# Kernel optimization log

Measured on AMD Instinct MI355X. Metric: run time of the kernel, lower is better.

The kernel has to match this reference:

```python
import jax, jax.numpy as jnp
import numpy as np

N = 50000      # nodes
E = 800000     # edges (avg degree 16)
IN = 256       # in_feats
H = 128        # hidden_feats
C = 40         # out_feats == num classes (label dim)
LPA_ITERS = 10


def setup_inputs() -> dict:
    key = jax.random.key(0)
    ks = jax.random.split(key, 9)
    features = jax.random.normal(ks[0], (N, IN), dtype=jnp.float32)
    labels = jax.random.normal(ks[1], (N, C), dtype=jnp.float32)
    mask = jax.random.randint(ks[2], (N,), 0, 2) > 0          # bool [N]
    src = jax.random.randint(ks[3], (E,), 0, N, dtype=jnp.int32)
    dst = jax.random.randint(ks[4], (E,), 0, N, dtype=jnp.int32)
    W1 = jax.random.normal(ks[5], (IN, H), dtype=jnp.float32) * (1.0 / np.sqrt(IN))
    b1 = jnp.zeros((H,), dtype=jnp.float32)
    W2 = jax.random.normal(ks[6], (H, C), dtype=jnp.float32) * (1.0 / np.sqrt(H))
    b2 = jnp.zeros((C,), dtype=jnp.float32)
    return {"features": features, "labels": labels, "mask": mask,
            "src": src, "dst": dst, "W1": W1, "b1": b1, "W2": W2, "b2": b2}


def reference(features, labels, mask, src, dst, W1, b1, W2, b2):
    ones_e = jnp.ones((E,), dtype=jnp.float32)
    deg_out = jax.ops.segment_sum(ones_e, src, num_segments=N)  # out-degree
    deg_in = jax.ops.segment_sum(ones_e, dst, num_segments=N)   # in-degree
    norm_src = jnp.maximum(deg_out, 1.0) ** -0.5                 # DGL clamps deg>=1
    norm_dst = jnp.maximum(deg_in, 1.0) ** -0.5

    def gconv(x, W, b):
        # DGL GraphConv, norm='both': D_in^{-1/2} A^T D_out^{-1/2} (x W) + b
        h = (x @ W) * norm_src[:, None]                          # [N, d_out]
        agg = jax.ops.segment_sum(h[src], dst, num_segments=N)   # gather+scatter-add
        return agg * norm_dst[:, None] + b

    x = jax.nn.relu(gconv(features, W1, b1))
    # dropout identity in eval mode
    x = gconv(x, W2, b2)

    # Label propagation: adj[src,dst]=1 so (adj @ y)[i] = sum_{(i->j)} y[j]
    masked_labels = jnp.where(mask[:, None], labels, 0.0)

    def step(y, _):
        y = jax.ops.segment_sum(y[dst], src, num_segments=N)
        y = jnp.where(mask[:, None], labels, y)
        return y, None

    y, _ = jax.lax.scan(step, masked_labels, None, length=LPA_ITERS)
    return x, y
```

## Files before the change

kernel.cpp:

```cpp
#include <hip/hip_runtime.h>

#define Nn 50000
#define Ee 800000
#define INF_ 256
#define HID 128
#define NC 40
#define CAPD 48
#define CAPS 48
#define LPA_ITERS 10
#define NB 98
#define BSH 9
#define EPB 1024
#define NBLK ((Ee + EPB - 1) / EPB)
#define G1_ROWS 64
#define G1BLK ((Nn + G1_ROWS - 1) / G1_ROWS)
#define CAPB_D 10240
#define CAPB_S 6144

typedef __attribute__((ext_vector_type(8))) short bfrag;
typedef __attribute__((ext_vector_type(4))) float ffrag;

__device__ inline unsigned f2bf2(float a, float b) {
    unsigned ua = __float_as_uint(a); ua += 0x7FFFu + ((ua >> 16) & 1u);
    unsigned ub = __float_as_uint(b); ub += 0x7FFFu + ((ub >> 16) & 1u);
    return (ua >> 16) | (ub & 0xFFFF0000u);
}
__device__ inline unsigned short f2bf(float a) {
    unsigned ua = __float_as_uint(a); ua += 0x7FFFu + ((ua >> 16) & 1u);
    return (unsigned short)(ua >> 16);
}
__device__ inline float bf_lo(unsigned u) { return __uint_as_float(u << 16); }
__device__ inline float bf_hi(unsigned u) { return __uint_as_float(u & 0xFFFF0000u); }

__global__ void detect_fmt(const unsigned int* __restrict__ m, int* flag) {
    int i = blockIdx.x * blockDim.x + threadIdx.x;
    if (i < 12500) {
        if (m[i] > 1u) atomicOr(flag, 1);
    }
}

__device__ inline bool read_mask(const void* mask, int node, int fmt) {
    if (fmt) return ((const unsigned char*)mask)[node] != 0;
    return ((const int*)mask)[node] != 0;
}

__global__ void prep_w1t(const float* __restrict__ W1,
                         unsigned short* __restrict__ W1t) {
    int c = blockIdx.x;
    int k = threadIdx.x;
    W1t[c * INF_ + k] = f2bf(W1[(size_t)k * HID + c]);
}

__global__ __launch_bounds__(256) void phase1(
    const int* __restrict__ src, const int* __restrict__ dst,
    const void* __restrict__ mask, const int* __restrict__ flag,
    int* __restrict__ cnt_src, int* __restrict__ cur_d, int* __restrict__ cur_s,
    unsigned* __restrict__ bkt_d, unsigned* __restrict__ bkt_s,
    const float* __restrict__ feat, const unsigned short* __restrict__ W1t,
    unsigned short* __restrict__ h1b) {
    __shared__ uint4 smem[784];
    const int tid = threadIdx.x;
    if (blockIdx.x < NBLK) {
        unsigned* stage_d = (unsigned*)smem;
        unsigned* stage_s = stage_d + EPB;
        int* hd  = (int*)(stage_s + EPB);
        int* od  = hd + NB;
        int* cd  = od + NB + 1;
        int* gd_ = cd + NB;
        int* hs  = gd_ + NB;
        int* os_ = hs + NB;
        int* cs_ = os_ + NB + 1;
        int* gs_ = cs_ + NB;
        int lane = tid & 63;
        int wid = tid >> 6;
        int e0 = blockIdx.x * EPB;
        int fmt = *flag;
        if (tid < NB) { hd[tid] = 0; hs[tid] = 0; }
        __syncthreads();

        int rs[EPB / 256], rd[EPB / 256];
        unsigned um = 0;
#pragma unroll
        for (int k = 0; k < EPB / 256; k++) {
            int e = e0 + tid + k * 256;
            rs[k] = -1; rd[k] = -1;
            if (e < Ee) {
                int s = src[e], d = dst[e];
                rs[k] = s; rd[k] = d;
                atomicAdd(&cnt_src[s], 1);
                atomicAdd(&hd[d >> BSH], 1);
                if (!read_mask(mask, s, fmt)) {
                    um |= (1u << k);
                    atomicAdd(&hs[s >> BSH], 1);
                }
            }
        }
        __syncthreads();
        if (wid < 2) {
            int* h = wid ? hs : hd;
            int* o = wid ? os_ : od;
            int i0 = lane * 2;
            int v0 = (i0 < NB) ? h[i0] : 0;
            int v1 = (i0 + 1 < NB) ? h[i0 + 1] : 0;
            int s = v0 + v1;
#pragma unroll
            for (int d = 1; d < 64; d <<= 1) {
                int t = __shfl_up(s, d);
                if (lane >= d) s += t;
            }
            int excl = s - v0 - v1;
            if (i0 < NB) o[i0] = excl;
            if (i0 + 1 < NB) o[i0 + 1] = excl + v0;
            if (lane == 63) o[NB] = s;
        }
        __syncthreads();
        if (tid < NB) {
            gd_[tid] = hd[tid] ? atomicAdd(&cur_d[tid], hd[tid]) : 0;
            gs_[tid] = hs[tid] ? atomicAdd(&cur_s[tid], hs[tid]) : 0;
            cd[tid] = od[tid];
            cs_[tid] = os_[tid];
        }
        __syncthreads();
#pragma unroll
        for (int k = 0; k < EPB / 256; k++) {
            if (rd[k] >= 0) {
                int p = atomicAdd(&cd[rd[k] >> BSH], 1);
                stage_d[p] = ((unsigned)rd[k] << 16) | (unsigned)rs[k];
                if (um & (1u << k)) {
                    int q = atomicAdd(&cs_[rs[k] >> BSH], 1);
                    stage_s[q] = ((unsigned)rs[k] << 16) | (unsigned)rd[k];
                }
            }
        }
        __syncthreads();
        for (int b = wid; b < NB; b += 4) {
            int base = od[b], cntb = hd[b], g0 = gd_[b];
            unsigned* gb = bkt_d + (size_t)b * CAPB_D;
            for (int i = lane; i < cntb; i += 64) {
                int pos = g0 + i;
                if (pos < CAPB_D) gb[pos] = stage_d[base + i];
            }
            int bs = os_[b], cnts = hs[b], gs0 = gs_[b];
            unsigned* gbs = bkt_s + (size_t)b * CAPB_S;
            for (int i = lane; i < cnts; i += 64) {
                int pos = gs0 + i;
                if (pos < CAPB_S) gbs[pos] = stage_s[bs + i];
            }
        }
    } else {
        unsigned short* lA = (unsigned short*)smem;
        unsigned short* lB = lA + G1_ROWS * 32;
        const int row0 = (blockIdx.x - NBLK) * G1_ROWS;
        const int w = tid >> 6;
        const int l = tid & 63;
        const int lane15 = l & 15;
        const int quad = l >> 4;
        const int rw0 = w * 16;

        ffrag acc[8];
#pragma unroll
        for (int t = 0; t < 8; t++) acc[t] = (ffrag){0.f, 0.f, 0.f, 0.f};

        for (int k0 = 0; k0 < INF_; k0 += 32) {
#pragma unroll
            for (int p = 0; p < 2; p++) {
                int idx = tid + p * 256;
                int r = idx >> 3, c4 = idx & 7;
                int grow = row0 + r;
                float4 v = make_float4(0.f, 0.f, 0.f, 0.f);
                if (grow < Nn)
                    v = *(const float4*)(feat + (size_t)grow * INF_ + k0 + c4 * 4);
                uint2 pk;
                pk.x = f2bf2(v.x, v.y);
                pk.y = f2bf2(v.z, v.w);
                *(uint2*)((char*)lA + r * 64 + c4 * 8) = pk;
            }
#pragma unroll
            for (int p = 0; p < 2; p++) {
                int idx = tid + p * 256;
                int col = idx >> 2, q = idx & 3;
                uint4 v = *(const uint4*)((const char*)W1t + col * 512 + k0 * 2 + q * 16);
                *(uint4*)((char*)lB + col * 64 + q * 16) = v;
            }
            __syncthreads();
            int arow = rw0 + lane15;
            bfrag af = *(const bfrag*)((const char*)lA + arow * 64 + quad * 16);
#pragma unroll
            for (int t = 0; t < 8; t++) {
                int col = t * 16 + lane15;
                bfrag bf = *(const bfrag*)((const char*)lB + col * 64 + quad * 16);
                acc[t] = __builtin_amdgcn_mfma_f32_16x16x32_bf16(af, bf, acc[t], 0, 0, 0);
            }
            __syncthreads();
        }
#pragma unroll
        for (int t = 0; t < 8; t++) {
#pragma unroll
            for (int i = 0; i < 4; i++) {
                int grow = row0 + rw0 + quad * 4 + i;
                if (grow < Nn)
                    h1b[(size_t)grow * HID + t * 16 + lane15] = f2bf(acc[t][i]);
            }
        }
    }
}

__global__ __launch_bounds__(256) void build_csr_both(
    const unsigned* __restrict__ bkt_d, const int* __restrict__ cur_d,
    const unsigned* __restrict__ bkt_s, const int* __restrict__ cur_s,
    const void* __restrict__ mask, const int* __restrict__ flag,
    const int* __restrict__ cnt_src,
    int* __restrict__ adj_dst, int* __restrict__ cnt_dst,
    int* __restrict__ adj_s, int* __restrict__ cnt_u, int* __restrict__ cnt_m,
    float* __restrict__ nrm_s, int* __restrict__ n_un, int* __restrict__ ulist) {
    __shared__ int lu[512], lm[512];
    int bb = blockIdx.x, tid = threadIdx.x;
    lu[tid] = 0; lu[tid + 256] = 0; lm[tid] = 0; lm[tid + 256] = 0;
    __syncthreads();
    if (bb < NB) {
        int b = bb;
        int n = cur_d[b]; if (n > CAPB_D) n = CAPB_D;
        int n0 = b << BSH;
        const unsigned* base = bkt_d + (size_t)b * CAPB_D;
        for (int i = tid; i < n; i += 256) {
            unsigned r = base[i];
            int d = r >> 16, s = r & 0xffff;
            int sl = atomicAdd(&lu[d - n0], 1);
            if (sl < CAPD) adj_dst[d * CAPD + sl] = s;
        }
        __syncthreads();
        int g0 = n0 + tid;
        if (g0 < Nn) cnt_dst[g0] = lu[tid];
        g0 += 256;
        if (g0 < Nn) cnt_dst[g0] = lu[tid + 256];
    } else {
        int b = bb - NB;
        int fmt = *flag;
        int n = cur_s[b]; if (n > CAPB_S) n = CAPB_S;
        int n0 = b << BSH;
        const unsigned* base = bkt_s + (size_t)b * CAPB_S;
        for (int i = tid; i < n; i += 256) {
            unsigned r = base[i];
            int s = r >> 16, d = r & 0xffff;
            if (read_mask(mask, d, fmt)) {
                int sl = atomicAdd(&lm[s - n0], 1);
                if (sl < CAPS) adj_s[s * CAPS + (CAPS - 1 - sl)] = d;
            } else {
                int sl = atomicAdd(&lu[s - n0], 1);
                if (sl < CAPS) adj_s[s * CAPS + sl] = d;
            }
        }
        __syncthreads();
        int g0 = n0 + tid;
        if (g0 < Nn) {
            cnt_u[g0] = lu[tid]; cnt_m[g0] = lm[tid];
            int cs = cnt_src[g0];
            nrm_s[g0] = rsqrtf((float)(cs > 1 ? cs : 1));
            if (!read_mask(mask, g0, fmt)) {
                int p = atomicAdd(n_un, 1);
                ulist[p] = g0;
            }
        }
        g0 += 256;
        if (g0 < Nn) {
            cnt_u[g0] = lu[tid + 256]; cnt_m[g0] = lm[tid + 256];
            int cs = cnt_src[g0];
            nrm_s[g0] = rsqrtf((float)(cs > 1 ? cs : 1));
            if (!read_mask(mask, g0, fmt)) {
                int p = atomicAdd(n_un, 1);
                ulist[p] = g0;
            }
        }
    }
}

__global__ __launch_bounds__(256) void agg_relu1(
    const uint4* __restrict__ h1b, const int* __restrict__ adj_dst,
    const int* __restrict__ cnt_dst, const float* __restrict__ nrm_s,
    const float4* __restrict__ b1, float4* __restrict__ x1) {
    int node = blockIdx.x * 16 + (threadIdx.x >> 4);
    int l = threadIdx.x & 15;
    int dg = cnt_dst[node];
    int cnt = dg < CAPD ? dg : CAPD;
    const int* lst = adj_dst + (size_t)node * CAPD;
    float s0 = 0.f, s1 = 0.f, s2 = 0.f, s3 = 0.f;
    float s4 = 0.f, s5 = 0.f, s6 = 0.f, s7 = 0.f;
    int e = 0;
    for (; e + 8 <= cnt; e += 8) {
        uint4 u[8]; float ns[8];
#pragma unroll
        for (int q = 0; q < 8; q++) {
            int sidx = lst[e + q];
            u[q] = h1b[(size_t)sidx * 16 + l];
            ns[q] = nrm_s[sidx];
        }
#pragma unroll
        for (int q = 0; q < 8; q++) {
            s0 += ns[q] * bf_lo(u[q].x); s1 += ns[q] * bf_hi(u[q].x);
            s2 += ns[q] * bf_lo(u[q].y); s3 += ns[q] * bf_hi(u[q].y);
            s4 += ns[q] * bf_lo(u[q].z); s5 += ns[q] * bf_hi(u[q].z);
            s6 += ns[q] * bf_lo(u[q].w); s7 += ns[q] * bf_hi(u[q].w);
        }
    }
    for (; e < cnt; e++) {
        int sidx = lst[e];
        uint4 u = h1b[(size_t)sidx * 16 + l];
        float nsv = nrm_s[sidx];
        s0 += nsv * bf_lo(u.x); s1 += nsv * bf_hi(u.x);
        s2 += nsv * bf_lo(u.y); s3 += nsv * bf_hi(u.y);
        s4 += nsv * bf_lo(u.z); s5 += nsv * bf_hi(u.z);
        s6 += nsv * bf_lo(u.w); s7 += nsv * bf_hi(u.w);
    }
    float nrm = rsqrtf((float)(dg > 1 ? dg : 1));
    float4 bb0 = b1[l * 2], bb1 = b1[l * 2 + 1];
    float4 v0, v1;
    v0.x = fmaxf(s0 * nrm + bb0.x, 0.f);
    v0.y = fmaxf(s1 * nrm + bb0.y, 0.f);
    v0.z = fmaxf(s2 * nrm + bb0.z, 0.f);
    v0.w = fmaxf(s3 * nrm + bb0.w, 0.f);
    v1.x = fmaxf(s4 * nrm + bb1.x, 0.f);
    v1.y = fmaxf(s5 * nrm + bb1.y, 0.f);
    v1.z = fmaxf(s6 * nrm + bb1.z, 0.f);
    v1.w = fmaxf(s7 * nrm + bb1.w, 0.f);
    x1[(size_t)node * 32 + l * 2] = v0;
    x1[(size_t)node * 32 + l * 2 + 1] = v1;
}

__global__ __launch_bounds__(256) void gemm2(
    const float4* __restrict__ x1, const float4* __restrict__ W2,
    const int* __restrict__ cnt_src, unsigned* __restrict__ h2b) {
    __shared__ float lw[HID * NC];
    int tid = threadIdx.x;
    for (int i = tid; i < HID * NC / 4; i += 256)
        ((float4*)lw)[i] = W2[i];
    __syncthreads();
    int r = blockIdx.x * 256 + tid;
    if (r >= Nn) return;
    const float4* xr = x1 + (size_t)r * 32;
    float4 acc[10];
#pragma unroll
    for (int j = 0; j < 10; j++) acc[j] = make_float4(0.f, 0.f, 0.f, 0.f);
    for (int k4 = 0; k4 < 32; k4++) {
        float4 xv = xr[k4];
#pragma unroll
        for (int s = 0; s < 4; s++) {
            float x = s == 0 ? xv.x : (s == 1 ? xv.y : (s == 2 ? xv.z : xv.w));
            const float4* wrow = (const float4*)(lw + (k4 * 4 + s) * NC);
#pragma unroll
            for (int j = 0; j < 10; j++) {
                float4 w = wrow[j];
                acc[j].x += x * w.x; acc[j].y += x * w.y;
                acc[j].z += x * w.z; acc[j].w += x * w.w;
            }
        }
    }
    int dg = cnt_src[r];
    float nrm = rsqrtf((float)(dg > 1 ? dg : 1));
    uint2* out = (uint2*)(h2b + (size_t)r * 20);
#pragma unroll
    for (int j = 0; j < 10; j++) {
        uint2 pk;
        pk.x = f2bf2(acc[j].x * nrm, acc[j].y * nrm);
        pk.y = f2bf2(acc[j].z * nrm, acc[j].w * nrm);
        out[j] = pk;
    }
}

__global__ __launch_bounds__(320) void agg2(
    const uint2* __restrict__ h2b, const int* __restrict__ adj_dst,
    const int* __restrict__ cnt_dst, const float4* __restrict__ b2,
    float4* __restrict__ out_x) {
    int node = blockIdx.x * 32 + threadIdx.x / 10;
    int l = threadIdx.x % 10;
    if (node >= Nn) return;
    int dg = cnt_dst[node];
    int cnt = dg < CAPD ? dg : CAPD;
    const int* lst = adj_dst + (size_t)node * CAPD;
    float s0 = 0.f, s1 = 0.f, s2 = 0.f, s3 = 0.f;
    int e = 0;
    for (; e + 8 <= cnt; e += 8) {
        uint2 u[8];
#pragma unroll
        for (int q = 0; q < 8; q++) u[q] = h2b[(size_t)lst[e + q] * 10 + l];
#pragma unroll
        for (int q = 0; q < 8; q++) {
            s0 += bf_lo(u[q].x); s1 += bf_hi(u[q].x);
            s2 += bf_lo(u[q].y); s3 += bf_hi(u[q].y);
        }
    }
    for (; e + 4 <= cnt; e += 4) {
        uint2 u[4];
#pragma unroll
        for (int q = 0; q < 4; q++) u[q] = h2b[(size_t)lst[e + q] * 10 + l];
#pragma unroll
        for (int q = 0; q < 4; q++) {
            s0 += bf_lo(u[q].x); s1 += bf_hi(u[q].x);
            s2 += bf_lo(u[q].y); s3 += bf_hi(u[q].y);
        }
    }
    for (; e < cnt; e++) {
        uint2 u = h2b[(size_t)lst[e] * 10 + l];
        s0 += bf_lo(u.x); s1 += bf_hi(u.x);
        s2 += bf_lo(u.y); s3 += bf_hi(u.y);
    }
    float nrm = rsqrtf((float)(dg > 1 ? dg : 1));
    float4 bb = b2[l];
    float4 v;
    v.x = s0 * nrm + bb.x;
    v.y = s1 * nrm + bb.y;
    v.z = s2 * nrm + bb.z;
    v.w = s3 * nrm + bb.w;
    out_x[(size_t)node * 10 + l] = v;
}

__global__ __launch_bounds__(320) void lpa_const(
    const float4* __restrict__ labels, const void* __restrict__ mask,
    const int* __restrict__ flag, const int* __restrict__ n_un,
    const int* __restrict__ ulist, const int* __restrict__ adj_s,
    const int* __restrict__ cnt_m, float4* __restrict__ sconst,
    uint2* __restrict__ y1b, float4* __restrict__ out_y4) {
    int fmt = *flag;
    int i = blockIdx.x * 320 + threadIdx.x;
    if (i < Nn * 10) {
        int node = i / 10;
        if (read_mask(mask, node, fmt)) out_y4[i] = labels[i];
    }
    int g = blockIdx.x * 32 + threadIdx.x / 10;
    int l = threadIdx.x % 10;
    if (g >= *n_un) return;
    int u = ulist[g];
    int cm = cnt_m[u];
    int cnt = cm < CAPS ? cm : CAPS;
    const int* lst = adj_s + (size_t)u * CAPS + (CAPS - cnt);
    float4 s = make_float4(0.f, 0.f, 0.f, 0.f);
    int e = 0;
    for (; e + 8 <= cnt; e += 8) {
        float4 v[8];
#pragma unroll
        for (int q = 0; q < 8; q++) v[q] = labels[(size_t)lst[e + q] * 10 + l];
#pragma unroll
        for (int q = 0; q < 8; q++) {
            s.x += v[q].x; s.y += v[q].y; s.z += v[q].z; s.w += v[q].w;
        }
    }
    for (; e + 4 <= cnt; e += 4) {
        float4 v[4];
#pragma unroll
        for (int q = 0; q < 4; q++) v[q] = labels[(size_t)lst[e + q] * 10 + l];
#pragma unroll
        for (int q = 0; q < 4; q++) {
            s.x += v[q].x; s.y += v[q].y; s.z += v[q].z; s.w += v[q].w;
        }
    }
    for (; e < cnt; e++) {
        float4 a = labels[(size_t)lst[e] * 10 + l];
        s.x += a.x; s.y += a.y; s.z += a.z; s.w += a.w;
    }
    sconst[(size_t)u * 10 + l] = s;
    uint2 pk; pk.x = f2bf2(s.x, s.y); pk.y = f2bf2(s.z, s.w);
    y1b[(size_t)u * 10 + l] = pk;
}

__global__ __launch_bounds__(320) void lpa_mid(
    const uint2* __restrict__ ycur, const int* __restrict__ n_un,
    const int* __restrict__ ulist, const int* __restrict__ adj_s,
    const int* __restrict__ cnt_u, const float4* __restrict__ sconst,
    uint2* __restrict__ ynext) {
    int g = blockIdx.x * 32 + threadIdx.x / 10;
    int l = threadIdx.x % 10;
    if (g >= *n_un) return;
    int u = ulist[g];
    int cu = cnt_u[u];
    int cnt = cu < CAPS ? cu : CAPS;
    const int* lst = adj_s + (size_t)u * CAPS;
    float4 s = sconst[(size_t)u * 10 + l];
    int e = 0;
    for (; e + 8 <= cnt; e += 8) {
        uint2 v[8];
#pragma unroll
        for (int q = 0; q < 8; q++) v[q] = ycur[(size_t)lst[e + q] * 10 + l];
#pragma unroll
        for (int q = 0; q < 8; q++) {
            s.x += bf_lo(v[q].x); s.y += bf_hi(v[q].x);
            s.z += bf_lo(v[q].y); s.w += bf_hi(v[q].y);
        }
    }
    for (; e + 4 <= cnt; e += 4) {
        uint2 v[4];
#pragma unroll
        for (int q = 0; q < 4; q++) v[q] = ycur[(size_t)lst[e + q] * 10 + l];
#pragma unroll
        for (int q = 0; q < 4; q++) {
            s.x += bf_lo(v[q].x); s.y += bf_hi(v[q].x);
            s.z += bf_lo(v[q].y); s.w += bf_hi(v[q].y);
        }
    }
    for (; e < cnt; e++) {
        uint2 v = ycur[(size_t)lst[e] * 10 + l];
        s.x += bf_lo(v.x); s.y += bf_hi(v.x);
        s.z += bf_lo(v.y); s.w += bf_hi(v.y);
    }
    uint2 pk; pk.x = f2bf2(s.x, s.y); pk.y = f2bf2(s.z, s.w);
    ynext[(size_t)u * 10 + l] = pk;
}

__global__ __launch_bounds__(320) void lpa_last(
    const uint2* __restrict__ ycur, const int* __restrict__ n_un,
    const int* __restrict__ ulist, const int* __restrict__ adj_s,
    const int* __restrict__ cnt_u, const float4* __restrict__ sconst,
    float4* __restrict__ out_y) {
    int g = blockIdx.x * 32 + threadIdx.x / 10;
    int l = threadIdx.x % 10;
    if (g >= *n_un) return;
    int u = ulist[g];
    int cu = cnt_u[u];
    int cnt = cu < CAPS ? cu : CAPS;
    const int* lst = adj_s + (size_t)u * CAPS;
    float4 s = sconst[(size_t)u * 10 + l];
    int e = 0;
    for (; e + 8 <= cnt; e += 8) {
        uint2 v[8];
#pragma unroll
        for (int q = 0; q < 8; q++) v[q] = ycur[(size_t)lst[e + q] * 10 + l];
#pragma unroll
        for (int q = 0; q < 8; q++) {
            s.x += bf_lo(v[q].x); s.y += bf_hi(v[q].x);
            s.z += bf_lo(v[q].y); s.w += bf_hi(v[q].y);
        }
    }
    for (; e + 4 <= cnt; e += 4) {
        uint2 v[4];
#pragma unroll
        for (int q = 0; q < 4; q++) v[q] = ycur[(size_t)lst[e + q] * 10 + l];
#pragma unroll
        for (int q = 0; q < 4; q++) {
            s.x += bf_lo(v[q].x); s.y += bf_hi(v[q].x);
            s.z += bf_lo(v[q].y); s.w += bf_hi(v[q].y);
        }
    }
    for (; e < cnt; e++) {
        uint2 v = ycur[(size_t)lst[e] * 10 + l];
        s.x += bf_lo(v.x); s.y += bf_hi(v.x);
        s.z += bf_lo(v.y); s.w += bf_hi(v.y);
    }
    out_y[(size_t)u * 10 + l] = s;
}

extern "C" void kernel_launch(void* const* d_in, const int* in_sizes, int n_in,
                              void* d_out, int out_size, void* d_ws, size_t ws_size,
                              hipStream_t stream) {
    const float* feat   = (const float*)d_in[0];
    const float* labels = (const float*)d_in[1];
    const void*  mask   = d_in[2];
    const int*   src    = (const int*)d_in[3];
    const int*   dst    = (const int*)d_in[4];
    const float* W1     = (const float*)d_in[5];
    const float* b1     = (const float*)d_in[6];
    const float* W2     = (const float*)d_in[7];
    const float* b2     = (const float*)d_in[8];

    float* out_x = (float*)d_out;
    float* out_y = out_x + (size_t)Nn * NC;

    char* ws = (char*)d_ws;
    size_t off = 0;
    auto alloc = [&](size_t bytes) -> void* {
        void* p = ws + off;
        off += (bytes + 255) & ~(size_t)255;
        return p;
    };
    int* flag    = (int*)alloc(256);
    int* n_un    = flag + 1;
    int* cnt_src = (int*)alloc((size_t)Nn * 4);
    int* cur_d   = (int*)alloc(512);
    int* cur_s   = (int*)alloc(512);
    size_t zero_bytes = off;
    int* cnt_dst = (int*)alloc((size_t)Nn * 4);
    int* cnt_u   = (int*)alloc((size_t)Nn * 4);
    int* cnt_m   = (int*)alloc((size_t)Nn * 4);
    int* ulist   = (int*)alloc((size_t)Nn * 4);
    float* nrm_s = (float*)alloc((size_t)Nn * 4);
    unsigned short* W1t = (unsigned short*)alloc((size_t)HID * INF_ * 2);
    unsigned* bkt_d = (unsigned*)alloc((size_t)NB * CAPB_D * 4);
    unsigned* bkt_s = (unsigned*)alloc((size_t)NB * CAPB_S * 4);
    unsigned short* h1b = (unsigned short*)alloc((size_t)Nn * HID * 2);
    float* x1 = (float*)alloc((size_t)Nn * HID * 4);
    int* adj_s   = (int*)alloc((size_t)Nn * CAPS * 4);
    int* adj_dst = (int*)alloc((size_t)Nn * CAPD * 4);
    unsigned* h2b = (unsigned*)alloc((size_t)Nn * NC * 2);
    float* sconst = (float*)alloc((size_t)Nn * NC * 4);
    uint2* y1b = (uint2*)alloc((size_t)Nn * NC * 2);
    uint2* y2b = (uint2*)alloc((size_t)Nn * NC * 2);

    hipMemsetAsync(d_ws, 0, zero_bytes, stream);

    detect_fmt<<<49, 256, 0, stream>>>((const unsigned int*)mask, flag);
    prep_w1t<<<HID, INF_, 0, stream>>>(W1, W1t);
    phase1<<<NBLK + G1BLK, 256, 0, stream>>>(
        src, dst, mask, flag, cnt_src, cur_d, cur_s, bkt_d, bkt_s,
        feat, W1t, h1b);
    build_csr_both<<<NB * 2, 256, 0, stream>>>(
        bkt_d, cur_d, bkt_s, cur_s, mask, flag, cnt_src,
        adj_dst, cnt_dst, adj_s, cnt_u, cnt_m, nrm_s, n_un, ulist);

    agg_relu1<<<Nn / 16, 256, 0, stream>>>((const uint4*)h1b, adj_dst, cnt_dst,
                                           nrm_s, (const float4*)b1, (float4*)x1);
    gemm2<<<196, 256, 0, stream>>>((const float4*)x1, (const float4*)W2,
                                   cnt_src, h2b);
    agg2<<<(Nn + 31) / 32, 320, 0, stream>>>((const uint2*)h2b, adj_dst, cnt_dst,
                                             (const float4*)b2, (float4*)out_x);

    lpa_const<<<(Nn + 31) / 32, 320, 0, stream>>>(
        (const float4*)labels, mask, flag, n_un, ulist, adj_s, cnt_m,
        (float4*)sconst, y1b, (float4*)out_y);
    const uint2* cur = y1b;
    for (int i = 0; i < 8; i++) {
        uint2* nxt = (i & 1) ? y1b : y2b;
        lpa_mid<<<(Nn + 31) / 32, 320, 0, stream>>>(
            cur, n_un, ulist, adj_s, cnt_u, (const float4*)sconst, nxt);
        cur = nxt;
    }
    lpa_last<<<(Nn + 31) / 32, 320, 0, stream>>>(
        cur, n_un, ulist, adj_s, cnt_u, (const float4*)sconst, (float4*)out_y);
}
```

Measured before the change: 380.4 us.

## Co-schedule GCN layer kernels with independent LPA iterations via block-range fusion

Measured after the change: 375.1 us. About the same (-1.4%).

```diff
diff --git a/kernel.cpp b/kernel.cpp
--- a/kernel.cpp
+++ b/kernel.cpp
@@ -16,6 +16,9 @@
 #define G1BLK ((Nn + G1_ROWS - 1) / G1_ROWS)
 #define CAPB_D 10240
 #define CAPB_S 6144
+#define AGG1_BLKS 2500
+#define LPA_BLKS ((Nn + 31) / 32)
+#define GEMM2_BLKS ((Nn + 319) / 320)
 
 typedef __attribute__((ext_vector_type(8))) short bfrag;
 typedef __attribute__((ext_vector_type(4))) float ffrag;
@@ -32,23 +35,24 @@
 __device__ inline float bf_lo(unsigned u) { return __uint_as_float(u << 16); }
 __device__ inline float bf_hi(unsigned u) { return __uint_as_float(u & 0xFFFF0000u); }
 
-__global__ void detect_fmt(const unsigned int* __restrict__ m, int* flag) {
-    int i = blockIdx.x * blockDim.x + threadIdx.x;
-    if (i < 12500) {
-        if (m[i] > 1u) atomicOr(flag, 1);
-    }
-}
-
 __device__ inline bool read_mask(const void* mask, int node, int fmt) {
     if (fmt) return ((const unsigned char*)mask)[node] != 0;
     return ((const int*)mask)[node] != 0;
 }
 
-__global__ void prep_w1t(const float* __restrict__ W1,
-                         unsigned short* __restrict__ W1t) {
-    int c = blockIdx.x;
-    int k = threadIdx.x;
-    W1t[c * INF_ + k] = f2bf(W1[(size_t)k * HID + c]);
+__global__ __launch_bounds__(256) void detect_prep(
+    const unsigned int* __restrict__ m, int* flag,
+    const float* __restrict__ W1, unsigned short* __restrict__ W1t) {
+    int bb = blockIdx.x, tid = threadIdx.x;
+    if (bb < 49) {
+        int i = bb * 256 + tid;
+        if (i < 12500) {
+            if (m[i] > 1u) atomicOr(flag, 1);
+        }
+    } else {
+        int c = bb - 49;
+        W1t[c * INF_ + tid] = f2bf(W1[(size_t)tid * HID + c]);
+    }
 }
 
 __global__ __launch_bounds__(256) void phase1(
@@ -274,12 +278,12 @@
     }
 }
 
-__global__ __launch_bounds__(256) void agg_relu1(
-    const uint4* __restrict__ h1b, const int* __restrict__ adj_dst,
-    const int* __restrict__ cnt_dst, const float* __restrict__ nrm_s,
-    const float4* __restrict__ b1, float4* __restrict__ x1) {
-    int node = blockIdx.x * 16 + (threadIdx.x >> 4);
-    int l = threadIdx.x & 15;
+
+__device__ inline void do_agg1(
+    int node, int l, const uint4* __restrict__ h1b,
+    const int* __restrict__ adj_dst, const int* __restrict__ cnt_dst,
+    const float* __restrict__ nrm_s, const float4* __restrict__ b1,
+    float4* __restrict__ x1) {
     int dg = cnt_dst[node];
     int cnt = dg < CAPD ? dg : CAPD;
     const int* lst = adj_dst + (size_t)node * CAPD;
@@ -326,53 +330,88 @@
     x1[(size_t)node * 32 + l * 2 + 1] = v1;
 }
 
-__global__ __launch_bounds__(256) void gemm2(
-    const float4* __restrict__ x1, const float4* __restrict__ W2,
-    const int* __restrict__ cnt_src, unsigned* __restrict__ h2b) {
-    __shared__ float lw[HID * NC];
-    int tid = threadIdx.x;
-    for (int i = tid; i < HID * NC / 4; i += 256)
-        ((float4*)lw)[i] = W2[i];
-    __syncthreads();
-    int r = blockIdx.x * 256 + tid;
-    if (r >= Nn) return;
-    const float4* xr = x1 + (size_t)r * 32;
-    float4 acc[10];
-#pragma unroll
-    for (int j = 0; j < 10; j++) acc[j] = make_float4(0.f, 0.f, 0.f, 0.f);
-    for (int k4 = 0; k4 < 32; k4++) {
-        float4 xv = xr[k4];
-#pragma unroll
-        for (int s = 0; s < 4; s++) {
-            float x = s == 0 ? xv.x : (s == 1 ? xv.y : (s == 2 ? xv.z : xv.w));
-            const float4* wrow = (const float4*)(lw + (k4 * 4 + s) * NC);
-#pragma unroll
-            for (int j = 0; j < 10; j++) {
-                float4 w = wrow[j];
-                acc[j].x += x * w.x; acc[j].y += x * w.y;
-                acc[j].z += x * w.z; acc[j].w += x * w.w;
-            }
-        }
-    }
-    int dg = cnt_src[r];
-    float nrm = rsqrtf((float)(dg > 1 ? dg : 1));
-    uint2* out = (uint2*)(h2b + (size_t)r * 20);
-#pragma unroll
-    for (int j = 0; j < 10; j++) {
-        uint2 pk;
-        pk.x = f2bf2(acc[j].x * nrm, acc[j].y * nrm);
-        pk.y = f2bf2(acc[j].z * nrm, acc[j].w * nrm);
-        out[j] = pk;
-    }
-}
-
-__global__ __launch_bounds__(320) void agg2(
-    const uint2* __restrict__ h2b, const int* __restrict__ adj_dst,
-    const int* __restrict__ cnt_dst, const float4* __restrict__ b2,
-    float4* __restrict__ out_x) {
-    int node = blockIdx.x * 32 + threadIdx.x / 10;
-    int l = threadIdx.x % 10;
-    if (node >= Nn) return;
+__device__ inline void do_lpa_const(
+    int g, int l, const float4* __restrict__ labels,
+    const int* __restrict__ ulist, const int* __restrict__ adj_s,
+    const int* __restrict__ cnt_m, float4* __restrict__ sconst,
+    uint2* __restrict__ y1b) {
+    int u = ulist[g];
+    int cm = cnt_m[u];
+    int cnt = cm < CAPS ? cm : CAPS;
+    const int* lst = adj_s + (size_t)u * CAPS + (CAPS - cnt);
+    float4 s = make_float4(0.f, 0.f, 0.f, 0.f);
+    int e = 0;
+    for (; e + 8 <= cnt; e += 8) {
+        float4 v[8];
+#pragma unroll
+        for (int q = 0; q < 8; q++) v[q] = labels[(size_t)lst[e + q] * 10 + l];
+#pragma unroll
+        for (int q = 0; q < 8; q++) {
+            s.x += v[q].x; s.y += v[q].y; s.z += v[q].z; s.w += v[q].w;
+        }
+    }
+    for (; e + 4 <= cnt; e += 4) {
+        float4 v[4];
+#pragma unroll
+        for (int q = 0; q < 4; q++) v[q] = labels[(size_t)lst[e + q] * 10 + l];
+#pragma unroll
+        for (int q = 0; q < 4; q++) {
+            s.x += v[q].x; s.y += v[q].y; s.z += v[q].z; s.w += v[q].w;
+        }
+    }
+    for (; e < cnt; e++) {
+        float4 a = labels[(size_t)lst[e] * 10 + l];
+        s.x += a.x; s.y += a.y; s.z += a.z; s.w += a.w;
+    }
+    sconst[(size_t)u * 10 + l] = s;
+    uint2 pk; pk.x = f2bf2(s.x, s.y); pk.y = f2bf2(s.z, s.w);
+    y1b[(size_t)u * 10 + l] = pk;
+}
+
+__device__ inline void do_lpa_mid(
+    int g, int l, const uint2* __restrict__ ycur,
+    const int* __restrict__ ulist, const int* __restrict__ adj_s,
+    const int* __restrict__ cnt_u, const float4* __restrict__ sconst,
+    uint2* __restrict__ ynext) {
+    int u = ulist[g];
+    int cu = cnt_u[u];
+    int cnt = cu < CAPS ? cu : CAPS;
+    const int* lst = adj_s + (size_t)u * CAPS;
+    float4 s = sconst[(size_t)u * 10 + l];
+    int e = 0;
+    for (; e + 8 <= cnt; e += 8) {
+        uint2 v[8];
+#pragma unroll
+        for (int q = 0; q < 8; q++) v[q] = ycur[(size_t)lst[e + q] * 10 + l];
+#pragma unroll
+        for (int q = 0; q < 8; q++) {
+            s.x += bf_lo(v[q].x); s.y += bf_hi(v[q].x);
+            s.z += bf_lo(v[q].y); s.w += bf_hi(v[q].y);
+        }
+    }
+    for (; e + 4 <= cnt; e += 4) {
+        uint2 v[4];
+#pragma unroll
+        for (int q = 0; q < 4; q++) v[q] = ycur[(size_t)lst[e + q] * 10 + l];
+#pragma unroll
+        for (int q = 0; q < 4; q++) {
+            s.x += bf_lo(v[q].x); s.y += bf_hi(v[q].x);
+            s.z += bf_lo(v[q].y); s.w += bf_hi(v[q].y);
+        }
+    }
+    for (; e < cnt; e++) {
+        uint2 v = ycur[(size_t)lst[e] * 10 + l];
+        s.x += bf_lo(v.x); s.y += bf_hi(v.x);
+        s.z += bf_lo(v.y); s.w += bf_hi(v.y);
+    }
+    uint2 pk; pk.x = f2bf2(s.x, s.y); pk.y = f2bf2(s.z, s.w);
+    ynext[(size_t)u * 10 + l] = pk;
+}
+
+__device__ inline void do_agg2(
+    int node, int l, const uint2* __restrict__ h2b,
+    const int* __restrict__ adj_dst, const int* __restrict__ cnt_dst,
+    const float4* __restrict__ b2, float4* __restrict__ out_x) {
     int dg = cnt_dst[node];
     int cnt = dg < CAPD ? dg : CAPD;
     const int* lst = adj_dst + (size_t)node * CAPD;
@@ -413,52 +452,101 @@
     out_x[(size_t)node * 10 + l] = v;
 }
 
-__global__ __launch_bounds__(320) void lpa_const(
+__global__ __launch_bounds__(320) void k_agg1_lconst(
+    const uint4* __restrict__ h1b, const int* __restrict__ adj_dst,
+    const int* __restrict__ cnt_dst, const float* __restrict__ nrm_s,
+    const float4* __restrict__ b1, float4* __restrict__ x1,
     const float4* __restrict__ labels, const void* __restrict__ mask,
     const int* __restrict__ flag, const int* __restrict__ n_un,
     const int* __restrict__ ulist, const int* __restrict__ adj_s,
     const int* __restrict__ cnt_m, float4* __restrict__ sconst,
     uint2* __restrict__ y1b, float4* __restrict__ out_y4) {
-    int fmt = *flag;
-    int i = blockIdx.x * 320 + threadIdx.x;
-    if (i < Nn * 10) {
-        int node = i / 10;
-        if (read_mask(mask, node, fmt)) out_y4[i] = labels[i];
-    }
-    int g = blockIdx.x * 32 + threadIdx.x / 10;
-    int l = threadIdx.x % 10;
-    if (g >= *n_un) return;
-    int u = ulist[g];
-    int cm = cnt_m[u];
-    int cnt = cm < CAPS ? cm : CAPS;
-    const int* lst = adj_s + (size_t)u * CAPS + (CAPS - cnt);
-    float4 s = make_float4(0.f, 0.f, 0.f, 0.f);
-    int e = 0;
-    for (; e + 8 <= cnt; e += 8) {
-        float4 v[8];
-#pragma unroll
-        for (int q = 0; q < 8; q++) v[q] = labels[(size_t)lst[e + q] * 10 + l];
-#pragma unroll
-        for (int q = 0; q < 8; q++) {
-            s.x += v[q].x; s.y += v[q].y; s.z += v[q].z; s.w += v[q].w;
-        }
-    }
-    for (; e + 4 <= cnt; e += 4) {
-        float4 v[4];
-#pragma unroll
-        for (int q = 0; q < 4; q++) v[q] = labels[(size_t)lst[e + q] * 10 + l];
-#pragma unroll
-        for (int q = 0; q < 4; q++) {
-            s.x += v[q].x; s.y += v[q].y; s.z += v[q].z; s.w += v[q].w;
-        }
-    }
-    for (; e < cnt; e++) {
-        float4 a = labels[(size_t)lst[e] * 10 + l];
-        s.x += a.x; s.y += a.y; s.z += a.z; s.w += a.w;
-    }
-    sconst[(size_t)u * 10 + l] = s;
-    uint2 pk; pk.x = f2bf2(s.x, s.y); pk.y = f2bf2(s.z, s.w);
-    y1b[(size_t)u * 10 + l] = pk;
+    int bb = blockIdx.x, tid = threadIdx.x;
+    if (bb < AGG1_BLKS) {
+        int node = bb * 20 + (tid >> 4);
+        do_agg1(node, tid & 15, h1b, adj_dst, cnt_dst, nrm_s, b1, x1);
+    } else {
+        int lb = bb - AGG1_BLKS;
+        int fmt = *flag;
+        int i = lb * 320 + tid;
+        if (i < Nn * 10) {
+            int node = i / 10;
+            if (read_mask(mask, node, fmt)) out_y4[i] = labels[i];
+        }
+        int g = lb * 32 + tid / 10;
+        if (g < *n_un)
+            do_lpa_const(g, tid % 10, labels, ulist, adj_s, cnt_m, sconst, y1b);
+    }
+}
+
+__global__ __launch_bounds__(320) void k_gemm2_mid(
+    const float4* __restrict__ x1, const float4* __restrict__ W2,
+    const int* __restrict__ cnt_src, unsigned* __restrict__ h2b,
+    const uint2* __restrict__ ycur, const int* __restrict__ n_un,
+    const int* __restrict__ ulist, const int* __restrict__ adj_s,
+    const int* __restrict__ cnt_u, const float4* __restrict__ sconst,
+    uint2* __restrict__ ynext) {
+    __shared__ float lw[HID * NC];
+    int bb = blockIdx.x, tid = threadIdx.x;
+    if (bb < GEMM2_BLKS) {
+        for (int i = tid; i < HID * NC / 4; i += 320)
+            ((float4*)lw)[i] = W2[i];
+        __syncthreads();
+        int r = bb * 320 + tid;
+        if (r >= Nn) return;
+        const float4* xr = x1 + (size_t)r * 32;
+        float4 acc[10];
+#pragma unroll
+        for (int j = 0; j < 10; j++) acc[j] = make_float4(0.f, 0.f, 0.f, 0.f);
+        for (int k4 = 0; k4 < 32; k4++) {
+            float4 xv = xr[k4];
+#pragma unroll
+            for (int s = 0; s < 4; s++) {
+                float x = s == 0 ? xv.x : (s == 1 ? xv.y : (s == 2 ? xv.z : xv.w));
+                const float4* wrow = (const float4*)(lw + (k4 * 4 + s) * NC);
+#pragma unroll
+                for (int j = 0; j < 10; j++) {
+                    float4 w = wrow[j];
+                    acc[j].x += x * w.x; acc[j].y += x * w.y;
+                    acc[j].z += x * w.z; acc[j].w += x * w.w;
+                }
+            }
+        }
+        int dg = cnt_src[r];
+        float nrm = rsqrtf((float)(dg > 1 ? dg : 1));
+        uint2* out = (uint2*)(h2b + (size_t)r * 20);
+#pragma unroll
+        for (int j = 0; j < 10; j++) {
+            uint2 pk;
+            pk.x = f2bf2(acc[j].x * nrm, acc[j].y * nrm);
+            pk.y = f2bf2(acc[j].z * nrm, acc[j].w * nrm);
+            out[j] = pk;
+        }
+    } else {
+        int g = (bb - GEMM2_BLKS) * 32 + tid / 10;
+        if (g < *n_un)
+            do_lpa_mid(g, tid % 10, ycur, ulist, adj_s, cnt_u, sconst, ynext);
+    }
+}
+
+__global__ __launch_bounds__(320) void k_agg2_mid(
+    const uint2* __restrict__ h2b, const int* __restrict__ adj_dst,
+    const int* __restrict__ cnt_dst, const float4* __restrict__ b2,
+    float4* __restrict__ out_x,
+    const uint2* __restrict__ ycur, const int* __restrict__ n_un,
+    const int* __restrict__ ulist, const int* __restrict__ adj_s,
+    const int* __restrict__ cnt_u, const float4* __restrict__ sconst,
+    uint2* __restrict__ ynext) {
+    int bb = blockIdx.x, tid = threadIdx.x;
+    if (bb < LPA_BLKS) {
+        int node = bb * 32 + tid / 10;
+        if (node < Nn)
+            do_agg2(node, tid % 10, h2b, adj_dst, cnt_dst, b2, out_x);
+    } else {
+        int g = (bb - LPA_BLKS) * 32 + tid / 10;
+        if (g < *n_un)
+            do_lpa_mid(g, tid % 10, ycur, ulist, adj_s, cnt_u, sconst, ynext);
+    }
 }
 
 __global__ __launch_bounds__(320) void lpa_mid(
@@ -467,41 +555,8 @@
     const int* __restrict__ cnt_u, const float4* __restrict__ sconst,
     uint2* __restrict__ ynext) {
     int g = blockIdx.x * 32 + threadIdx.x / 10;
-    int l = threadIdx.x % 10;
-    if (g >= *n_un) return;
-    int u = ulist[g];
-    int cu = cnt_u[u];
-    int cnt = cu < CAPS ? cu : CAPS;
-    const int* lst = adj_s + (size_t)u * CAPS;
-    float4 s = sconst[(size_t)u * 10 + l];
-    int e = 0;
-    for (; e + 8 <= cnt; e += 8) {
-        uint2 v[8];
-#pragma unroll
-        for (int q = 0; q < 8; q++) v[q] = ycur[(size_t)lst[e + q] * 10 + l];
-#pragma unroll
-        for (int q = 0; q < 8; q++) {
-            s.x += bf_lo(v[q].x); s.y += bf_hi(v[q].x);
-            s.z += bf_lo(v[q].y); s.w += bf_hi(v[q].y);
-        }
-    }
-    for (; e + 4 <= cnt; e += 4) {
-        uint2 v[4];
-#pragma unroll
-        for (int q = 0; q < 4; q++) v[q] = ycur[(size_t)lst[e + q] * 10 + l];
-#pragma unroll
-        for (int q = 0; q < 4; q++) {
-            s.x += bf_lo(v[q].x); s.y += bf_hi(v[q].x);
-            s.z += bf_lo(v[q].y); s.w += bf_hi(v[q].y);
-        }
-    }
-    for (; e < cnt; e++) {
-        uint2 v = ycur[(size_t)lst[e] * 10 + l];
-        s.x += bf_lo(v.x); s.y += bf_hi(v.x);
-        s.z += bf_lo(v.y); s.w += bf_hi(v.y);
-    }
-    uint2 pk; pk.x = f2bf2(s.x, s.y); pk.y = f2bf2(s.z, s.w);
-    ynext[(size_t)u * 10 + l] = pk;
+    if (g < *n_un)
+        do_lpa_mid(g, threadIdx.x % 10, ycur, ulist, adj_s, cnt_u, sconst, ynext);
 }
 
 __global__ __launch_bounds__(320) void lpa_last(
@@ -594,8 +649,8 @@
 
     hipMemsetAsync(d_ws, 0, zero_bytes, stream);
 
-    detect_fmt<<<49, 256, 0, stream>>>((const unsigned int*)mask, flag);
-    prep_w1t<<<HID, INF_, 0, stream>>>(W1, W1t);
+    detect_prep<<<49 + HID, 256, 0, stream>>>((const unsigned int*)mask, flag,
+                                              W1, W1t);
     phase1<<<NBLK + G1BLK, 256, 0, stream>>>(
         src, dst, mask, flag, cnt_src, cur_d, cur_s, bkt_d, bkt_s,
         feat, W1t, h1b);
@@ -603,23 +658,24 @@
         bkt_d, cur_d, bkt_s, cur_s, mask, flag, cnt_src,
         adj_dst, cnt_dst, adj_s, cnt_u, cnt_m, nrm_s, n_un, ulist);
 
-    agg_relu1<<<Nn / 16, 256, 0, stream>>>((const uint4*)h1b, adj_dst, cnt_dst,
-                                           nrm_s, (const float4*)b1, (float4*)x1);
-    gemm2<<<196, 256, 0, stream>>>((const float4*)x1, (const float4*)W2,
-                                   cnt_src, h2b);
-    agg2<<<(Nn + 31) / 32, 320, 0, stream>>>((const uint2*)h2b, adj_dst, cnt_dst,
-                                             (const float4*)b2, (float4*)out_x);
-
-    lpa_const<<<(Nn + 31) / 32, 320, 0, stream>>>(
-        (const float4*)labels, mask, flag, n_un, ulist, adj_s, cnt_m,
-        (float4*)sconst, y1b, (float4*)out_y);
+    k_agg1_lconst<<<AGG1_BLKS + LPA_BLKS, 320, 0, stream>>>(
+        (const uint4*)h1b, adj_dst, cnt_dst, nrm_s, (const float4*)b1,
+        (float4*)x1, (const float4*)labels, mask, flag, n_un, ulist, adj_s,
+        cnt_m, (float4*)sconst, y1b, (float4*)out_y);
+    k_gemm2_mid<<<GEMM2_BLKS + LPA_BLKS, 320, 0, stream>>>(
+        (const float4*)x1, (const float4*)W2, cnt_src, h2b,
+        y1b, n_un, ulist, adj_s, cnt_u, (const float4*)sconst, y2b);
+    k_agg2_mid<<<LPA_BLKS + LPA_BLKS, 320, 0, stream>>>(
+        (const uint2*)h2b, adj_dst, cnt_dst, (const float4*)b2, (float4*)out_x,
+        y2b, n_un, ulist, adj_s, cnt_u, (const float4*)sconst, y1b);
+
     const uint2* cur = y1b;
-    for (int i = 0; i < 8; i++) {
+    for (int i = 0; i < 6; i++) {
         uint2* nxt = (i & 1) ? y1b : y2b;
-        lpa_mid<<<(Nn + 31) / 32, 320, 0, stream>>>(
+        lpa_mid<<<LPA_BLKS, 320, 0, stream>>>(
             cur, n_un, ulist, adj_s, cnt_u, (const float4*)sconst, nxt);
         cur = nxt;
     }
-    lpa_last<<<(Nn + 31) / 32, 320, 0, stream>>>(
+    lpa_last<<<LPA_BLKS, 320, 0, stream>>>(
         cur, n_un, ulist, adj_s, cnt_u, (const float4*)sconst, (float4*)out_y);
 }
```
